# Performance work log

Hardware: AMD Instinct MI355X
Metric: run time of the kernel (lower is better)

The kernel has to match this reference:

```python
import jax, jax.numpy as jnp
import numpy as np

M, N = 24, 12
H1 = (M + N) * 10 * 8        # 2880
HID = (M * M + N * N) * 10   # 7200
H2 = M * N * 4               # 1152
DOUT = M * N                 # 288
EPS = 1e-12


def setup_inputs() -> dict:
    key = jax.random.key(0)
    ks = jax.random.split(key, 16)
    s = 0.02  # weight scale
    return {
        "yt": jax.random.normal(ks[0], (N,), jnp.float32),
        "F": jax.random.normal(ks[1], (M, M), jnp.float32) * 0.1,
        "Hm": jax.random.normal(ks[2], (N, M), jnp.float32) * 0.1,
        "m1x_posterior": jax.random.normal(ks[3], (M, 1), jnp.float32),
        "m1x_prior_old": jax.random.normal(ks[4], (M, 1), jnp.float32),
        "hn": jax.random.normal(ks[5], (HID,), jnp.float32),
        "W1": jax.random.normal(ks[6], (H1, M + N), jnp.float32) * s,
        "b1": jax.random.normal(ks[7], (H1,), jnp.float32) * s,
        "Wih": jax.random.normal(ks[8], (3 * HID, H1), jnp.float32) * s,
        "Whh": jax.random.normal(ks[9], (3 * HID, HID), jnp.float32) * s,
        "bih": jax.random.normal(ks[10], (3 * HID,), jnp.float32) * s,
        "bhh": jax.random.normal(ks[11], (3 * HID,), jnp.float32) * s,
        "W2": jax.random.normal(ks[12], (H2, HID), jnp.float32) * s,
        "b2": jax.random.normal(ks[13], (H2,), jnp.float32) * s,
        "W3": jax.random.normal(ks[14], (DOUT, H2), jnp.float32) * s,
        "b3": jax.random.normal(ks[15], (DOUT,), jnp.float32) * s,
    }


def _l2_normalize(x):
    # torch F.normalize(p=2, dim=0, eps=1e-12)
    return x / jnp.maximum(jnp.linalg.norm(x), EPS)


def _gru_cell(x, h, Wih, Whh, bih, bhh):
    gi = Wih @ x + bih            # [3*HID]
    gh = Whh @ h + bhh            # [3*HID]
    gi_r, gi_z, gi_n = jnp.split(gi, 3)
    gh_r, gh_z, gh_n = jnp.split(gh, 3)
    r = jax.nn.sigmoid(gi_r + gh_r)
    z = jax.nn.sigmoid(gi_z + gh_z)
    n = jnp.tanh(gi_n + r * gh_n)
    return (1.0 - z) * n + z * h


def reference(yt, F, Hm, m1x_posterior, m1x_prior_old, hn,
              W1, b1, Wih, Whh, bih, bhh, W2, b2, W3, b3):
    # step_prior
    m1x_prior = F @ m1x_posterior        # [M,1]
    m1y = Hm @ m1x_prior                 # [N,1]
    # step_KGain_est
    dm1x = _l2_normalize((m1x_posterior - m1x_prior_old)[:, 0])  # [M]
    dm1y = _l2_normalize(yt - m1y[:, 0])                         # [N]
    kg_in = jnp.concatenate([dm1y, dm1x])                        # [M+N]
    l1 = jax.nn.relu(W1 @ kg_in + b1)                            # [H1]
    h_new = _gru_cell(l1, hn, Wih, Whh, bih, bhh)                # [HID]
    l2 = jax.nn.relu(W2 @ h_new + b2)                            # [H2]
    kg = (W3 @ l2 + b3).reshape(M, N)                            # Kalman gain
    # KNet_step update
    dy = yt[:, None] - m1y                                       # [N,1]
    m1x_post_new = m1x_prior + kg @ dy                           # [M,1]
    return m1x_post_new[:, 0]
```

## Files before the change

### kernel.cpp

```cpp
#include <hip/hip_runtime.h>
#include <math.h>

#define M_DIM 24
#define N_DIM 12
#define H1    2880
#define HID   7200
#define H2    1152
#define DOUT  288
#define KGIN  (M_DIM + N_DIM)

#define WS_PRIOR 0
#define WS_DY    96
#define WS_L1    128
#define WS_HNEW  3072
#define WS_L2    10304
#define WS_GI    11520
#define WS_GH    33152
#define WS_GH2   54752

typedef float floatx4 __attribute__((ext_vector_type(4)));

__device__ __forceinline__ float wave_sum(float v) {
    #pragma unroll
    for (int o = 32; o; o >>= 1) v += __shfl_xor(v, o);
    return v;
}

__device__ __forceinline__ floatx4 ntload(const float4* p) {
    return __builtin_nontemporal_load((const floatx4*)p);
}

__global__ __launch_bounds__(256) void k_l1h(
        const float* __restrict__ yt, const float* __restrict__ F,
        const float* __restrict__ Hm, const float* __restrict__ post,
        const float* __restrict__ prior_old,
        const float* __restrict__ W1, const float* __restrict__ b1,
        float* __restrict__ ws) {
    __shared__ float s_prior[M_DIM];
    __shared__ float s_m1y[N_DIM];
    __shared__ float s_x[KGIN];
    __shared__ float s_dy[N_DIM];
    int t = threadIdx.x, lane = t & 63, w = t >> 6;

    if (t < M_DIM) {
        float acc = 0.f;
        #pragma unroll
        for (int j = 0; j < M_DIM; ++j) acc += F[t * M_DIM + j] * post[j];
        s_prior[t] = acc;
    }
    __syncthreads();
    if (t < N_DIM) {
        float acc = 0.f;
        #pragma unroll
        for (int j = 0; j < M_DIM; ++j) acc += Hm[t * M_DIM + j] * s_prior[j];
        s_m1y[t] = acc;
    }
    __syncthreads();
    if (w == 0) {
        float vx = 0.f;
        if (lane < M_DIM) vx = post[lane] - prior_old[lane];
        float nx = fmaxf(sqrtf(wave_sum(vx * vx)), 1e-12f);
        float vy = 0.f;
        if (lane < N_DIM) vy = yt[lane] - s_m1y[lane];
        float ny = fmaxf(sqrtf(wave_sum(vy * vy)), 1e-12f);
        if (lane < N_DIM) { s_x[lane] = vy / ny; s_dy[lane] = vy; }
        if (lane < M_DIM) s_x[N_DIM + lane] = vx / nx;
    }
    __syncthreads();

    if (blockIdx.x == 0) {
        if (t < M_DIM) ws[WS_PRIOR + t] = s_prior[t];
        if (t < N_DIM) ws[WS_DY + t] = s_dy[t];
    }

    int i = blockIdx.x * 4 + w;
    float acc = (lane < KGIN) ? W1[(size_t)i * KGIN + lane] * s_x[lane] : 0.f;
    acc = wave_sum(acc);
    if (lane == 0) ws[WS_L1 + i] = fmaxf(acc + b1[i], 0.f);
}

__global__ __launch_bounds__(256, 8) void k_gates(
        const float* __restrict__ Wih, const float* __restrict__ Whh,
        const float* __restrict__ bih, const float* __restrict__ bhh,
        const float* __restrict__ hn, float* __restrict__ ws) {
    int t = threadIdx.x, lane = t & 63, w = t >> 6;
    int b = blockIdx.x;
    int g = b >> 3, r = b & 7;
    int gm = g % 3;
    if (gm < 2) {
        int hb = ((g / 3) * 2 + gm) * 8 + r;
        int half = (hb >= 1800) ? 1 : 0;
        int Q = hb - half * 1800;
        int i = Q * 4 + w;
        int base = half * 900;
        const float4* xh = (const float4*)hn + base;
        const float4* ur = (const float4*)(Whh + (size_t)i * HID) + base;
        const float4* uz = (const float4*)(Whh + (size_t)(i + HID) * HID) + base;
        const float4* un = (const float4*)(Whh + (size_t)(i + 2 * HID) * HID) + base;
        float hr = 0.f, hz = 0.f, hh = 0.f;
        #pragma unroll 2
        for (int kk = 0; kk < 14; ++kk) {
            int k = kk * 64 + lane;
            float4 x = xh[k];
            floatx4 a = ntload(ur + k), bb = ntload(uz + k), c = ntload(un + k);
            hr += a.x * x.x + a.y * x.y + a.z * x.z + a.w * x.w;
            hz += bb.x * x.x + bb.y * x.y + bb.z * x.z + bb.w * x.w;
            hh += c.x * x.x + c.y * x.y + c.z * x.z + c.w * x.w;
        }
        if (lane < 4) {
            int k = 14 * 64 + lane;
            float4 x = xh[k];
            floatx4 a = ntload(ur + k), bb = ntload(uz + k), c = ntload(un + k);
            hr += a.x * x.x + a.y * x.y + a.z * x.z + a.w * x.w;
            hz += bb.x * x.x + bb.y * x.y + bb.z * x.z + bb.w * x.w;
            hh += c.x * x.x + c.y * x.y + c.z * x.z + c.w * x.w;
        }
        hr = wave_sum(hr); hz = wave_sum(hz); hh = wave_sum(hh);
        if (lane == 0) {
            if (half) {
                ws[WS_GH2 + i]           = hr;
                ws[WS_GH2 + HID + i]     = hz;
                ws[WS_GH2 + 2 * HID + i] = hh;
            } else {
                ws[WS_GH + i]           = hr + bhh[i];
                ws[WS_GH + HID + i]     = hz + bhh[i + HID];
                ws[WS_GH + 2 * HID + i] = hh + bhh[i + 2 * HID];
            }
        }
    } else {
        int i = ((g / 3) * 8 + r) * 4 + w;
        const float4* x1 = (const float4*)(ws + WS_L1);
        const float4* wr = (const float4*)(Wih + (size_t)i * H1);
        const float4* wz = (const float4*)(Wih + (size_t)(i + HID) * H1);
        const float4* wn = (const float4*)(Wih + (size_t)(i + 2 * HID) * H1);
        float ar = 0.f, az = 0.f, an = 0.f;
        #pragma unroll 2
        for (int kk = 0; kk < 11; ++kk) {
            int k = kk * 64 + lane;
            float4 x = x1[k];
            floatx4 a = ntload(wr + k), bb = ntload(wz + k), c = ntload(wn + k);
            ar += a.x * x.x + a.y * x.y + a.z * x.z + a.w * x.w;
            az += bb.x * x.x + bb.y * x.y + bb.z * x.z + bb.w * x.w;
            an += c.x * x.x + c.y * x.y + c.z * x.z + c.w * x.w;
        }
        if (lane < 16) {
            int k = 11 * 64 + lane;
            float4 x = x1[k];
            floatx4 a = ntload(wr + k), bb = ntload(wz + k), c = ntload(wn + k);
            ar += a.x * x.x + a.y * x.y + a.z * x.z + a.w * x.w;
            az += bb.x * x.x + bb.y * x.y + bb.z * x.z + bb.w * x.w;
            an += c.x * x.x + c.y * x.y + c.z * x.z + c.w * x.w;
        }
        ar = wave_sum(ar); az = wave_sum(az); an = wave_sum(an);
        if (lane == 0) {
            ws[WS_GI + i]           = ar + bih[i];
            ws[WS_GI + HID + i]     = az + bih[i + HID];
            ws[WS_GI + 2 * HID + i] = an + bih[i + 2 * HID];
        }
    }
}

__global__ __launch_bounds__(256) void k_comb(const float* __restrict__ hn,
                                              float* __restrict__ ws) {
    int i = blockIdx.x * 256 + threadIdx.x;
    if (i < HID) {
        float ghr = ws[WS_GH + i]           + ws[WS_GH2 + i];
        float ghz = ws[WS_GH + HID + i]     + ws[WS_GH2 + HID + i];
        float ghn = ws[WS_GH + 2 * HID + i] + ws[WS_GH2 + 2 * HID + i];
        float gr = ws[WS_GI + i] + ghr;
        float gz = ws[WS_GI + HID + i] + ghz;
        float r = 1.f / (1.f + expf(-gr));
        float z = 1.f / (1.f + expf(-gz));
        float n = tanhf(ws[WS_GI + 2 * HID + i] + r * ghn);
        ws[WS_HNEW + i] = (1.f - z) * n + z * hn[i];
    }
}

__global__ __launch_bounds__(256, 8) void k_l2(
        const float* __restrict__ W2, const float* __restrict__ b2,
        float* __restrict__ ws) {
    __shared__ float s_p[4];
    int t = threadIdx.x, lane = t & 63, w = t >> 6;
    int i = blockIdx.x;
    const float4* x4 = (const float4*)(ws + WS_HNEW);
    const float4* wr = (const float4*)(W2 + (size_t)i * HID);
    float acc = 0.f;
    #pragma unroll 2
    for (int kk = 0; kk < 7; ++kk) {
        int k = kk * 256 + t;
        float4 x = x4[k];
        float4 a = wr[k];
        acc += a.x * x.x + a.y * x.y + a.z * x.z + a.w * x.w;
    }
    if (t < 8) {
        int k = 7 * 256 + t;
        float4 x = x4[k];
        float4 a = wr[k];
        acc += a.x * x.x + a.y * x.y + a.z * x.z + a.w * x.w;
    }
    acc = wave_sum(acc);
    if (lane == 0) s_p[w] = acc;
    __syncthreads();
    if (t == 0)
        ws[WS_L2 + i] = fmaxf(s_p[0] + s_p[1] + s_p[2] + s_p[3] + b2[i], 0.f);
}

__global__ __launch_bounds__(768) void k_kg_out(
        const float* __restrict__ W3, const float* __restrict__ b3,
        const float* __restrict__ ws, float* __restrict__ out) {
    __shared__ float s_kg[N_DIM];
    int m = blockIdx.x;
    int t = threadIdx.x, lane = t & 63, w = t >> 6;
    int row = m * N_DIM + w;
    const float4* wr = (const float4*)(W3 + (size_t)row * H2);
    const float4* x4 = (const float4*)(ws + WS_L2);
    float acc = 0.f;
    #pragma unroll
    for (int kk = 0; kk < 4; ++kk) {
        int k = kk * 64 + lane;
        float4 x = x4[k];
        float4 a = wr[k];
        acc += a.x * x.x + a.y * x.y + a.z * x.z + a.w * x.w;
    }
    if (lane < 32) {
        int k = 4 * 64 + lane;
        float4 x = x4[k];
        float4 a = wr[k];
        acc += a.x * x.x + a.y * x.y + a.z * x.z + a.w * x.w;
    }
    acc = wave_sum(acc);
    if (lane == 0) s_kg[w] = acc + b3[row];
    __syncthreads();
    if (t == 0) {
        float a = ws[WS_PRIOR + m];
        #pragma unroll
        for (int n = 0; n < N_DIM; ++n) a += s_kg[n] * ws[WS_DY + n];
        out[m] = a;
    }
}

extern "C" void kernel_launch(void* const* d_in, const int* in_sizes, int n_in,
                              void* d_out, int out_size, void* d_ws, size_t ws_size,
                              hipStream_t stream) {
    const float* yt        = (const float*)d_in[0];
    const float* F         = (const float*)d_in[1];
    const float* Hm        = (const float*)d_in[2];
    const float* post      = (const float*)d_in[3];
    const float* prior_old = (const float*)d_in[4];
    const float* hn        = (const float*)d_in[5];
    const float* W1        = (const float*)d_in[6];
    const float* b1        = (const float*)d_in[7];
    const float* Wih       = (const float*)d_in[8];
    const float* Whh       = (const float*)d_in[9];
    const float* bih       = (const float*)d_in[10];
    const float* bhh       = (const float*)d_in[11];
    const float* W2        = (const float*)d_in[12];
    const float* b2        = (const float*)d_in[13];
    const float* W3        = (const float*)d_in[14];
    const float* b3        = (const float*)d_in[15];
    float* out = (float*)d_out;
    float* ws  = (float*)d_ws;

    k_l1h   <<<H1 / 4, 256, 0, stream>>>(yt, F, Hm, post, prior_old, W1, b1, ws);
    k_gates <<<5400, 256, 0, stream>>>(Wih, Whh, bih, bhh, hn, ws);
    k_comb  <<<(HID + 255) / 256, 256, 0, stream>>>(hn, ws);
    k_l2    <<<H2, 256, 0, stream>>>(W2, b2, ws);
    k_kg_out<<<M_DIM, 768, 0, stream>>>(W3, b3, ws, out);
}
```

Before: 157.2 us.

## Fuse L1 layer into gates kernel, recomputing it per Wih block in LDS

Removes the separate k_l1h launch. Each Wih-gate block in k_gates now recomputes the prior, the normalized inputs and the full 2880-element L1 activation into shared memory before its GRU input dot products. This drops one kernel launch and a global round-trip for l1. In exchange, each of the 1800 Wih blocks redoes the whole W1 matvec (about 400KB of W1 reads, mostly from cache) plus several barriers. The 11.5KB of shared memory per block may also reduce occupancy.

```diff
diff --git a/kernel.cpp b/kernel.cpp
--- a/kernel.cpp
+++ b/kernel.cpp
@@ -11,7 +11,6 @@
 
 #define WS_PRIOR 0
 #define WS_DY    96
-#define WS_L1    128
 #define WS_HNEW  3072
 #define WS_L2    10304
 #define WS_GI    11520
@@ -30,56 +29,11 @@
     return __builtin_nontemporal_load((const floatx4*)p);
 }
 
-__global__ __launch_bounds__(256) void k_l1h(
+__global__ __launch_bounds__(256, 8) void k_gates(
         const float* __restrict__ yt, const float* __restrict__ F,
         const float* __restrict__ Hm, const float* __restrict__ post,
         const float* __restrict__ prior_old,
         const float* __restrict__ W1, const float* __restrict__ b1,
-        float* __restrict__ ws) {
-    __shared__ float s_prior[M_DIM];
-    __shared__ float s_m1y[N_DIM];
-    __shared__ float s_x[KGIN];
-    __shared__ float s_dy[N_DIM];
-    int t = threadIdx.x, lane = t & 63, w = t >> 6;
-
-    if (t < M_DIM) {
-        float acc = 0.f;
-        #pragma unroll
-        for (int j = 0; j < M_DIM; ++j) acc += F[t * M_DIM + j] * post[j];
-        s_prior[t] = acc;
-    }
-    __syncthreads();
-    if (t < N_DIM) {
-        float acc = 0.f;
-        #pragma unroll
-        for (int j = 0; j < M_DIM; ++j) acc += Hm[t * M_DIM + j] * s_prior[j];
-        s_m1y[t] = acc;
-    }
-    __syncthreads();
-    if (w == 0) {
-        float vx = 0.f;
-        if (lane < M_DIM) vx = post[lane] - prior_old[lane];
-        float nx = fmaxf(sqrtf(wave_sum(vx * vx)), 1e-12f);
-        float vy = 0.f;
-        if (lane < N_DIM) vy = yt[lane] - s_m1y[lane];
-        float ny = fmaxf(sqrtf(wave_sum(vy * vy)), 1e-12f);
-        if (lane < N_DIM) { s_x[lane] = vy / ny; s_dy[lane] = vy; }
-        if (lane < M_DIM) s_x[N_DIM + lane] = vx / nx;
-    }
-    __syncthreads();
-
-    if (blockIdx.x == 0) {
-        if (t < M_DIM) ws[WS_PRIOR + t] = s_prior[t];
-        if (t < N_DIM) ws[WS_DY + t] = s_dy[t];
-    }
-
-    int i = blockIdx.x * 4 + w;
-    float acc = (lane < KGIN) ? W1[(size_t)i * KGIN + lane] * s_x[lane] : 0.f;
-    acc = wave_sum(acc);
-    if (lane == 0) ws[WS_L1 + i] = fmaxf(acc + b1[i], 0.f);
-}
-
-__global__ __launch_bounds__(256, 8) void k_gates(
         const float* __restrict__ Wih, const float* __restrict__ Whh,
         const float* __restrict__ bih, const float* __restrict__ bhh,
         const float* __restrict__ hn, float* __restrict__ ws) {
@@ -128,8 +82,63 @@
             }
         }
     } else {
+        __shared__ float s_prior[M_DIM];
+        __shared__ float s_m1y[N_DIM];
+        __shared__ float s_x[KGIN];
+        __shared__ float s_dy[N_DIM];
+        __shared__ float s_l1[H1];
+
+        if (t < M_DIM) {
+            float acc = 0.f;
+            #pragma unroll
+            for (int j = 0; j < M_DIM; ++j) acc += F[t * M_DIM + j] * post[j];
+            s_prior[t] = acc;
+        }
+        __syncthreads();
+        if (t < N_DIM) {
+            float acc = 0.f;
+            #pragma unroll
+            for (int j = 0; j < M_DIM; ++j) acc += Hm[t * M_DIM + j] * s_prior[j];
+            s_m1y[t] = acc;
+        }
+        __syncthreads();
+        if (w == 0) {
+            float vx = 0.f;
+            if (lane < M_DIM) vx = post[lane] - prior_old[lane];
+            float nx = fmaxf(sqrtf(wave_sum(vx * vx)), 1e-12f);
+            float vy = 0.f;
+            if (lane < N_DIM) vy = yt[lane] - s_m1y[lane];
+            float ny = fmaxf(sqrtf(wave_sum(vy * vy)), 1e-12f);
+            if (lane < N_DIM) { s_x[lane] = vy / ny; s_dy[lane] = vy; }
+            if (lane < M_DIM) s_x[N_DIM + lane] = vx / nx;
+        }
+        __syncthreads();
+
+        if (b == 16) {
+            if (t < M_DIM) ws[WS_PRIOR + t] = s_prior[t];
+            if (t < N_DIM) ws[WS_DY + t] = s_dy[t];
+        }
+
+        {
+            const float4* sx4 = (const float4*)s_x;
+            float4 xq[9];
+            #pragma unroll
+            for (int q = 0; q < 9; ++q) xq[q] = sx4[q];
+            for (int row = t; row < H1; row += 256) {
+                const float4* wrow = (const float4*)(W1 + (size_t)row * KGIN);
+                float acc = 0.f;
+                #pragma unroll
+                for (int q = 0; q < 9; ++q) {
+                    float4 a = wrow[q];
+                    acc += a.x * xq[q].x + a.y * xq[q].y + a.z * xq[q].z + a.w * xq[q].w;
+                }
+                s_l1[row] = fmaxf(acc + b1[row], 0.f);
+            }
+        }
+        __syncthreads();
+
         int i = ((g / 3) * 8 + r) * 4 + w;
-        const float4* x1 = (const float4*)(ws + WS_L1);
+        const float4* x1 = (const float4*)s_l1;
         const float4* wr = (const float4*)(Wih + (size_t)i * H1);
         const float4* wz = (const float4*)(Wih + (size_t)(i + HID) * H1);
         const float4* wn = (const float4*)(Wih + (size_t)(i + 2 * HID) * H1);
@@ -261,8 +270,8 @@
     float* out = (float*)d_out;
     float* ws  = (float*)d_ws;
 
-    k_l1h   <<<H1 / 4, 256, 0, stream>>>(yt, F, Hm, post, prior_old, W1, b1, ws);
-    k_gates <<<5400, 256, 0, stream>>>(Wih, Whh, bih, bhh, hn, ws);
+    k_gates <<<5400, 256, 0, stream>>>(yt, F, Hm, post, prior_old, W1, b1,
+                                       Wih, Whh, bih, bhh, hn, ws);
     k_comb  <<<(HID + 255) / 256, 256, 0, stream>>>(hn, ws);
     k_l2    <<<H2, 256, 0, stream>>>(W2, b2, ws);
     k_kg_out<<<M_DIM, 768, 0, stream>>>(W3, b3, ws, out);
```

After: 245.4 us. 56.1% more time.
